# Performance work log

Hardware: AMD Instinct MI355X
Metric: run time of the kernel (lower is better)

The kernel has to match this reference:

```python
import jax, jax.numpy as jnp
import numpy as np
from jax import lax

B = 8192
NQ = 4  # num_qubits
TWO_PI = 2.0 * np.pi
BN_EPS = 1e-5
ANG_EPS = 1e-6


def setup_inputs() -> dict:
    key = jax.random.key(0)
    ks = jax.random.split(key, 8)
    rn = lambda k, shape, s: jax.random.normal(k, shape, jnp.float32) * s
    return {
        "x": jax.random.normal(ks[0], (B, 1, 28, 28), jnp.float32),
        "conv1_w": rn(ks[1], (8, 1, 3, 3), 0.3),
        "conv1_b": jnp.zeros((8,), jnp.float32),
        "conv2_w": rn(ks[2], (16, 8, 3, 3), 0.1),
        "conv2_b": jnp.zeros((16,), jnp.float32),
        "fc1_w": rn(ks[3], (64, 16 * 7 * 7), 0.04),
        "fc1_b": jnp.zeros((64,), jnp.float32),
        "fc2_w": rn(ks[4], (NQ, 64), 0.12),
        "fc2_b": jnp.zeros((NQ,), jnp.float32),
        "bn_gamma": jnp.ones((NQ,), jnp.float32),
        "bn_beta": jnp.zeros((NQ,), jnp.float32),
        "var_params": jax.random.uniform(ks[5], (3 * NQ,), jnp.float32, 0.0, TWO_PI),
    }


# ---- batched 4-qubit statevector simulation (replaces per-sample Aer loop) ----

def _rx(t):
    c, s = jnp.cos(t / 2), jnp.sin(t / 2)
    return jnp.stack([jnp.stack([c + 0j, -1j * s], -1),
                      jnp.stack([-1j * s, c + 0j], -1)], -2).astype(jnp.complex64)


def _ry(t):
    c, s = jnp.cos(t / 2), jnp.sin(t / 2)
    return jnp.stack([jnp.stack([c, -s], -1),
                      jnp.stack([s, c], -1)], -2).astype(jnp.complex64)


def _rz(t):
    p = jnp.exp(-0.5j * t.astype(jnp.complex64))
    z = jnp.zeros_like(p)
    return jnp.stack([jnp.stack([p, z], -1),
                      jnp.stack([z, jnp.conj(p)], -1)], -2)


def _apply_1q(psi, U, q):
    # psi: [B, 2,2,2,2]; axis q+1 is qubit q. U: [2,2] or [B,2,2].
    psi = jnp.moveaxis(psi, q + 1, 1)
    if U.ndim == 2:
        psi = jnp.einsum('ij,bj...->bi...', U, psi)
    else:
        psi = jnp.einsum('bij,bj...->bi...', U, psi)
    return jnp.moveaxis(psi, 1, q + 1)


def _apply_cnot(psi, c, t):
    ac, at = c + 1, t + 1
    c0 = lax.index_in_dim(psi, 0, ac, keepdims=True)
    c1 = jnp.flip(lax.index_in_dim(psi, 1, ac, keepdims=True), axis=at)
    return jnp.concatenate([c0, c1], axis=ac)


def quantum_expectations(angles, var):
    # angles: [B, NQ] feature angles; var: [3*NQ] shared variational params.
    b = angles.shape[0]
    psi = jnp.zeros((b,) + (2,) * NQ, jnp.complex64)
    psi = psi.at[(slice(None),) + (0,) * NQ].set(1.0)
    for i in range(NQ):                       # Z feature map
        psi = _apply_1q(psi, _rz(angles[:, i]), i)
    for i in range(NQ):                       # RX/RY/RZ ansatz
        psi = _apply_1q(psi, _rx(var[3 * i]), i)
        psi = _apply_1q(psi, _ry(var[3 * i + 1]), i)
        psi = _apply_1q(psi, _rz(var[3 * i + 2]), i)
    for i in range(NQ - 1):                   # linear CNOT chain
        psi = _apply_cnot(psi, i, i + 1)
    p = psi.real ** 2 + psi.imag ** 2          # [B,2,2,2,2] probabilities
    exps = []
    for k in range(NQ):                       # <Z> on qubit k
        axes = tuple(a for a in range(1, NQ + 1) if a != k + 1)
        pk = jnp.sum(p, axis=axes)             # [B,2]
        exps.append(pk[:, 0] - pk[:, 1])
    expZ = jnp.stack(exps, axis=1)             # [B,NQ], qubit-indexed
    # Qiskit Pauli label 'I'*q+'Z'+'I'*(NQ-q-1) puts Z on qubit NQ-1-q -> reverse
    return expZ[:, ::-1]


def _forward(x, conv1_w, conv1_b, conv2_w, conv2_b, fc1_w, fc1_b,
             fc2_w, fc2_b, bn_gamma, bn_beta, var_params):
    dn = ('NCHW', 'OIHW', 'NCHW')
    h = lax.conv_general_dilated(x, conv1_w, (1, 1), 'SAME', dimension_numbers=dn)
    h = jax.nn.relu(h + conv1_b[None, :, None, None])
    h = lax.reduce_window(h, -jnp.inf, lax.max, (1, 1, 2, 2), (1, 1, 2, 2), 'VALID')
    h = lax.conv_general_dilated(h, conv2_w, (1, 1), 'SAME', dimension_numbers=dn)
    h = jax.nn.relu(h + conv2_b[None, :, None, None])
    h = lax.reduce_window(h, -jnp.inf, lax.max, (1, 1, 2, 2), (1, 1, 2, 2), 'VALID')
    feats = h.reshape(h.shape[0], -1)                         # [B, 16*7*7]
    h = jax.nn.relu(feats @ fc1_w.T + fc1_b)
    logits = h @ fc2_w.T + fc2_b                              # [B, NQ]
    # BatchNorm1d (training mode: biased batch stats)
    mu = jnp.mean(logits, axis=0)
    var = jnp.mean((logits - mu) ** 2, axis=0)
    cl = (logits - mu) / jnp.sqrt(var + BN_EPS) * bn_gamma + bn_beta
    # quantum branch is fully detached in the original (numpy round-trip)
    cld = lax.stop_gradient(cl)
    mn = jnp.min(cld, axis=1, keepdims=True)
    mx = jnp.max(cld, axis=1, keepdims=True)
    angles = (cld - mn) / (mx - mn + ANG_EPS) * TWO_PI
    q = lax.stop_gradient(quantum_expectations(angles, var_params))
    return cl + q


def reference(x, conv1_w, conv1_b, conv2_w, conv2_b, fc1_w, fc1_b,
              fc2_w, fc2_b, bn_gamma, bn_beta, var_params):
    return _forward(x, conv1_w, conv1_b, conv2_w, conv2_b, fc1_w, fc1_b,
                    fc2_w, fc2_b, bn_gamma, bn_beta, var_params)
```

## Files before the change

kernel.cpp:

```cpp
#include <hip/hip_runtime.h>
#include <math.h>
#include <stdint.h>

#define BATCH 8192
#define NS 8

typedef _Float16 f16;
typedef _Float16 f16x2 __attribute__((ext_vector_type(2)));
typedef _Float16 f16x8 __attribute__((ext_vector_type(8)));
typedef float f32x4 __attribute__((ext_vector_type(4)));
typedef uint32_t u32x4 __attribute__((ext_vector_type(4)));

__device__ __forceinline__ uint32_t pk2(float a, float b) {
    return __builtin_bit_cast(uint32_t, __builtin_amdgcn_cvt_pkrtz(a, b));
}
__device__ __forceinline__ uint32_t rfl_u(uint32_t v) {
    return (uint32_t)__builtin_amdgcn_readfirstlane((int)v);
}
__device__ __forceinline__ void wave_lds_fence() {
    asm volatile("s_waitcnt lgkmcnt(0)" ::: "memory");
}

__global__ __launch_bounds__(512) void fused_cnn(
    const float* __restrict__ x,
    const float* __restrict__ c1w,
    const float* __restrict__ c1b,
    const float* __restrict__ c2w,
    const float* __restrict__ c2b,
    const float* __restrict__ f1w,
    const float* __restrict__ f1b,
    const float* __restrict__ f2w,
    const float* __restrict__ f2b,
    float* __restrict__ logits)
{
    const int tid  = threadIdx.x;
    const int lane = tid & 63;
    const int wid  = tid >> 6;
    const int b0   = blockIdx.x * NS;

    __shared__ __align__(16) f16 h1[NS * 16 * 18 * 8];
    __shared__ __align__(16) unsigned char uni[NS * 1920];
    float* part = (float*)h1;
    float* shl  = (float*)((unsigned char*)h1 + 4096);

    {
        uint4 z = make_uint4(0, 0, 0, 0);
        uint4* zs = (uint4*)(uni + wid * 1920);
        for (int i = lane; i < 120; i += 64) zs[i] = z;
        uint4* zh = (uint4*)(h1 + wid * 2304);
        for (int i = lane; i < 288; i += 64) zh[i] = z;
    }

    f16x2 wpk[36], bpk[4];
#pragma unroll
    for (int t = 0; t < 9; ++t)
#pragma unroll
        for (int pr = 0; pr < 4; ++pr)
            wpk[t * 4 + pr] = __builtin_bit_cast(f16x2,
                rfl_u(pk2(c1w[(2 * pr) * 9 + t], c1w[(2 * pr + 1) * 9 + t])));
#pragma unroll
    for (int pr = 0; pr < 4; ++pr)
        bpk[pr] = __builtin_bit_cast(f16x2, rfl_u(pk2(c1b[2 * pr], c1b[2 * pr + 1])));

    const int col = lane & 15, grp = lane >> 4;

    f16x8 af[3];
#pragma unroll
    for (int st = 0; st < 3; ++st) {
        int tap = st * 4 + grp;
        if (tap < 9) {
            float tmp[8];
#pragma unroll
            for (int j = 0; j < 8; ++j) tmp[j] = c2w[(col * 8 + j) * 9 + tap];
            u32x4 t = { pk2(tmp[0], tmp[1]), pk2(tmp[2], tmp[3]),
                        pk2(tmp[4], tmp[5]), pk2(tmp[6], tmp[7]) };
            af[st] = __builtin_bit_cast(f16x8, t);
        } else {
            u32x4 t = {0u, 0u, 0u, 0u};
            af[st] = __builtin_bit_cast(f16x8, t);
        }
    }

    {
        f16* simg = (f16*)(uni + wid * 1920);
        const float* xb = x + (size_t)(b0 + wid) * 784;
        wave_lds_fence();
#pragma unroll 1
        for (int pass = 0; pass < 4; ++pass) {
            int item = pass * 64 + lane;
            if (item < 196) {
                int r = item / 7, c4 = item - 7 * r;
                float4 v = *(const float4*)(xb + r * 28 + c4 * 4);
                f16* dst = simg + (r + 1) * 32 + c4 * 4 + 1;
                dst[0] = (f16)v.x; dst[1] = (f16)v.y;
                dst[2] = (f16)v.z; dst[3] = (f16)v.w;
            }
        }
    }
    wave_lds_fence();

    {
        const f16* simg = (const f16*)(uni + wid * 1920);
        f16* h1s = h1 + wid * 2304;
#pragma unroll 1
        for (int pass = 0; pass < 4; ++pass) {
            int pix = pass * 64 + lane;
            if (pix < 196) {
                int py = pix / 14, px = pix - 14 * py;
                const f16* ib = simg + (2 * py) * 32 + 2 * px;
                f16x2 acc[2][2][4];
#pragma unroll
                for (int qy = 0; qy < 2; ++qy)
#pragma unroll
                for (int qx = 0; qx < 2; ++qx)
#pragma unroll
                for (int pr = 0; pr < 4; ++pr) acc[qy][qx][pr] = bpk[pr];

#pragma unroll
                for (int rr = 0; rr < 4; ++rr) {
                    f16x2 plo = *(const f16x2*)(ib + rr * 32);
                    f16x2 phi = *(const f16x2*)(ib + rr * 32 + 2);
                    f16x2 sp[4];
                    sp[0][0] = plo[0]; sp[0][1] = plo[0];
                    sp[1][0] = plo[1]; sp[1][1] = plo[1];
                    sp[2][0] = phi[0]; sp[2][1] = phi[0];
                    sp[3][0] = phi[1]; sp[3][1] = phi[1];
#pragma unroll
                    for (int qy = 0; qy < 2; ++qy) {
                        int ky = rr - qy;
                        if (ky < 0 || ky > 2) continue;
#pragma unroll
                        for (int qx = 0; qx < 2; ++qx)
#pragma unroll
                        for (int kx = 0; kx < 3; ++kx) {
#pragma unroll
                            for (int pr = 0; pr < 4; ++pr)
                                acc[qy][qx][pr] = __builtin_elementwise_fma(
                                    sp[qx + kx], wpk[(ky * 3 + kx) * 4 + pr],
                                    acc[qy][qx][pr]);
                        }
                    }
                }
                f16x2 z; z[0] = (f16)0.f; z[1] = (f16)0.f;
                uint32_t ov[4];
#pragma unroll
                for (int pr = 0; pr < 4; ++pr) {
                    f16x2 m = __builtin_elementwise_max(
                        __builtin_elementwise_max(acc[0][0][pr], acc[0][1][pr]),
                        __builtin_elementwise_max(acc[1][0][pr], acc[1][1][pr]));
                    m = __builtin_elementwise_max(m, z);
                    ov[pr] = __builtin_bit_cast(uint32_t, m);
                }
                uint4 val = make_uint4(ov[0], ov[1], ov[2], ov[3]);
                *(uint4*)(h1s + ((py + 1) * 18 + (px + 1)) * 8) = val;
            }
        }
    }
    wave_lds_fence();

    {
        const f16* h1b = h1 + wid * 2304;
        f16* sfeats = (f16*)uni + wid * 968;
        const int q = col & 3, pl = col >> 2;
        const int qy = q >> 1, qx = q & 1;
        int koff[3];
#pragma unroll
        for (int st = 0; st < 3; ++st) {
            int t = st * 4 + grp;
            int ky = (t < 9) ? (t / 3) : 0;
            int kx = (t < 9) ? (t - 3 * (t / 3)) : 0;
            koff[st] = (ky * 18 + kx) * 8;
        }
        f32x4 cb;
#pragma unroll
        for (int r = 0; r < 4; ++r) cb[r] = c2b[grp * 4 + r];

#pragma unroll 1
        for (int t = 0; t < 13; ++t) {
            int pc = 4 * t + pl; pc = pc > 48 ? 48 : pc;
            int py = (pc * 9363) >> 16;
            int px = pc - 7 * py;
            const f16* bp = h1b + ((2 * py + qy) * 18 + (2 * px + qx)) * 8;
            f32x4 c = cb;
#pragma unroll
            for (int st = 0; st < 3; ++st) {
                f16x8 bv = *(const f16x8*)(bp + koff[st]);
                c = __builtin_amdgcn_mfma_f32_16x16x32_f16(af[st], bv, c, 0, 0, 0);
            }
            float vr[4];
#pragma unroll
            for (int r = 0; r < 4; ++r) {
                float v = c[r];
                v = fmaxf(v, __shfl_xor(v, 1));
                v = fmaxf(v, __shfl_xor(v, 2));
                vr[r] = fmaxf(v, 0.f);
            }
            int p = 4 * t + pl;
            if (q == 0 && p <= 48) {
#pragma unroll
                for (int r = 0; r < 4; ++r)
                    sfeats[(grp * 4 + r) * 49 + p] = (f16)vr[r];
            }
        }
        if (lane < 8) *(uint32_t*)(sfeats + 784 + lane * 2) = 0u;
    }
    __syncthreads();

    {
        const int rt = wid & 3, kh = wid >> 2;
        const int row = rt * 16 + col;
        const float* wrow = f1w + (size_t)row * 784;
        const int kbase = kh * 416;
        const int steps = 13 - kh;
        const int scol = col < NS ? col : 0;
        const f16* fb = (const f16*)uni + scol * 968;
        f32x4 c = {0.f, 0.f, 0.f, 0.f};
#pragma unroll 4
        for (int st = 0; st < steps; ++st) {
            int k0 = kbase + st * 32 + grp * 8;
            f16x8 a;
            if (k0 < 784) {
                float4 lo = *(const float4*)(wrow + k0);
                float4 hi = *(const float4*)(wrow + k0 + 4);
                u32x4 t = { pk2(lo.x, lo.y), pk2(lo.z, lo.w),
                            pk2(hi.x, hi.y), pk2(hi.z, hi.w) };
                a = __builtin_bit_cast(f16x8, t);
            } else {
                u32x4 t = {0u, 0u, 0u, 0u};
                a = __builtin_bit_cast(f16x8, t);
            }
            f16x8 b = *(const f16x8*)(fb + k0);
            c = __builtin_amdgcn_mfma_f32_16x16x32_f16(a, b, c, 0, 0, 0);
        }
        if (col < NS) {
#pragma unroll
            for (int r = 0; r < 4; ++r)
                part[kh * 512 + (rt * 16 + grp * 4 + r) * 8 + col] = c[r];
        }
    }
    __syncthreads();

    {
        const int m = tid >> 3, sm = tid & 7;
        float v = part[m * 8 + sm] + part[512 + m * 8 + sm] + f1b[m];
        shl[sm * 64 + m] = fmaxf(v, 0.f);
    }
    __syncthreads();

    {
        float hv = shl[wid * 64 + lane];
        float lg[4];
#pragma unroll
        for (int o = 0; o < 4; ++o) {
            float pv = hv * f2w[o * 64 + lane];
#pragma unroll
            for (int sft = 32; sft >= 1; sft >>= 1) pv += __shfl_xor(pv, sft);
            lg[o] = pv + f2b[o];
        }
        if (lane == 0) {
            float4 out4 = make_float4(lg[0], lg[1], lg[2], lg[3]);
            *(float4*)(logits + (size_t)(b0 + wid) * 4) = out4;
        }
    }
}

__global__ __launch_bounds__(256) void stats_apply(
    const float* __restrict__ logits, const float* __restrict__ var,
    const float* __restrict__ gamma, const float* __restrict__ beta,
    float* __restrict__ out)
{
    const int tid = threadIdx.x;
    const float4* l4 = (const float4*)logits;

    float t[8] = {0, 0, 0, 0, 0, 0, 0, 0};
#pragma unroll 4
    for (int i = 0; i < 32; ++i) {
        float4 v = l4[tid + 256 * i];
        t[0] += v.x; t[1] += v.y; t[2] += v.z; t[3] += v.w;
        t[4] += v.x * v.x; t[5] += v.y * v.y; t[6] += v.z * v.z; t[7] += v.w * v.w;
    }
#pragma unroll
    for (int sft = 32; sft >= 1; sft >>= 1)
#pragma unroll
        for (int j = 0; j < 8; ++j) t[j] += __shfl_xor(t[j], sft);

    __shared__ float part[4][8];
    __shared__ float prm[8];
    if ((tid & 63) == 0) {
#pragma unroll
        for (int j = 0; j < 8; ++j) part[tid >> 6][j] = t[j];
    }
    __syncthreads();

    if (tid == 0) {
        float sums[8];
#pragma unroll
        for (int j = 0; j < 8; ++j)
            sums[j] = part[0][j] + part[1][j] + part[2][j] + part[3][j];

        float pr[16], pi[16];
#pragma unroll
        for (int i = 0; i < 16; ++i) { pr[i] = 0.f; pi[i] = 0.f; }
        pr[0] = 1.f;
        for (int q = 0; q < 4; ++q) {
            float a  = var[3 * q], b_ = var[3 * q + 1], c = var[3 * q + 2];
            float ca = cosf(0.5f * a),  sa = sinf(0.5f * a);
            float cb = cosf(0.5f * b_), sb = sinf(0.5f * b_);
            float cc = cosf(0.5f * c),  sc = sinf(0.5f * c);
            float m00r = cb * ca, m00i =  sb * sa;
            float m01r = -sb * ca, m01i = -cb * sa;
            float m10r =  sb * ca, m10i = -cb * sa;
            float m11r =  cb * ca, m11i = -sb * sa;
            float u00r = cc * m00r + sc * m00i, u00i = cc * m00i - sc * m00r;
            float u01r = cc * m01r + sc * m01i, u01i = cc * m01i - sc * m01r;
            float u10r = cc * m10r - sc * m10i, u10i = cc * m10i + sc * m10r;
            float u11r = cc * m11r - sc * m11i, u11i = cc * m11i + sc * m11r;
            int stq = 1 << (3 - q);
            for (int i = 0; i < 16; ++i) {
                if (i & stq) continue;
                int j = i | stq;
                float xr = pr[i], xi = pi[i], yr = pr[j], yi = pi[j];
                pr[i] = u00r * xr - u00i * xi + u01r * yr - u01i * yi;
                pi[i] = u00r * xi + u00i * xr + u01r * yi + u01i * yr;
                pr[j] = u10r * xr - u10i * xi + u11r * yr - u11i * yi;
                pi[j] = u10r * xi + u10i * xr + u11r * yi + u11i * yr;
            }
        }
        for (int c = 0; c < 3; ++c) {
            int scm = 1 << (3 - c), stm = 1 << (2 - c);
            for (int i = 0; i < 16; ++i) {
                if ((i & scm) && !(i & stm)) {
                    int j = i | stm;
                    float tr = pr[i], ti = pi[i];
                    pr[i] = pr[j]; pi[i] = pi[j];
                    pr[j] = tr;    pi[j] = ti;
                }
            }
        }
        float p[16];
#pragma unroll
        for (int i = 0; i < 16; ++i) p[i] = pr[i] * pr[i] + pi[i] * pi[i];
        float e[4];
        for (int k = 0; k < 4; ++k) {
            float s = 0.f;
            for (int i = 0; i < 16; ++i)
                s += ((i >> (3 - k)) & 1) ? -p[i] : p[i];
            e[k] = s;
        }
        const float invB = 1.0f / (float)BATCH;
        for (int j = 0; j < 4; ++j) {
            float mu   = sums[j] * invB;
            float vr   = sums[4 + j] * invB - mu * mu;
            float istd = 1.0f / sqrtf(vr + 1e-5f);
            float scale = gamma[j] * istd;
            prm[j]     = scale;
            prm[4 + j] = beta[j] - mu * scale + e[3 - j];
        }
    }
    __syncthreads();

    const int smp = blockIdx.x * 256 + tid;
    float4 v = l4[smp];
    float4 r;
    r.x = v.x * prm[0] + prm[4];
    r.y = v.y * prm[1] + prm[5];
    r.z = v.z * prm[2] + prm[6];
    r.w = v.w * prm[3] + prm[7];
    ((float4*)out)[smp] = r;
}

extern "C" void kernel_launch(void* const* d_in, const int* in_sizes, int n_in,
                              void* d_out, int out_size, void* d_ws, size_t ws_size,
                              hipStream_t stream) {
    (void)in_sizes; (void)n_in; (void)out_size; (void)ws_size;
    const float* x   = (const float*)d_in[0];
    const float* c1w = (const float*)d_in[1];
    const float* c1b = (const float*)d_in[2];
    const float* c2w = (const float*)d_in[3];
    const float* c2b = (const float*)d_in[4];
    const float* f1w = (const float*)d_in[5];
    const float* f1b = (const float*)d_in[6];
    const float* f2w = (const float*)d_in[7];
    const float* f2b = (const float*)d_in[8];
    const float* gma = (const float*)d_in[9];
    const float* bta = (const float*)d_in[10];
    const float* var = (const float*)d_in[11];
    float* out = (float*)d_out;

    float* logits = (float*)d_ws;

    fused_cnn<<<BATCH / NS, 512, 0, stream>>>(x, c1w, c1b, c2w, c2b,
                                              f1w, f1b, f2w, f2b, logits);
    stats_apply<<<32, 256, 0, stream>>>(logits, var, gma, bta, out);
}
```

Before: 146.7 us.

## Prepack fc1 weights to fp16, halve samples per block, restructure conv2 pooling

Adds a small pre-kernel that converts fc1 weights to zero-padded fp16 once per call, so the fused kernel loads packed halves instead of converting fp32 on every block. The block shrinks to 4 samples and 256 threads, with an occupancy hint. Each wave now computes all 64 fc1 outputs for its row tile over the full K range, which removes the split-K partial buffer and one barrier. Conv2 now computes all four pooling quadrants per MFMA tile and takes the max in registers, replacing the cross-lane shuffles. Image staging is also widened to packed 32-bit stores. The trade-off is an extra kernel launch and fc1 weight reads repeated across twice as many blocks.

```diff
diff --git a/kernel.cpp b/kernel.cpp
--- a/kernel.cpp
+++ b/kernel.cpp
@@ -3,7 +3,7 @@
 #include <stdint.h>
 
 #define BATCH 8192
-#define NS 8
+#define NS 4
 
 typedef _Float16 f16;
 typedef _Float16 f16x2 __attribute__((ext_vector_type(2)));
@@ -21,13 +21,26 @@
     asm volatile("s_waitcnt lgkmcnt(0)" ::: "memory");
 }
 
-__global__ __launch_bounds__(512) void fused_cnn(
+__global__ __launch_bounds__(256) void pack_weights(
+    const float* __restrict__ f1w, uint32_t* __restrict__ w1p16)
+{
+    int idx = blockIdx.x * 256 + threadIdx.x;
+    if (idx < 25600) {
+        int o = idx / 400, pos = idx - o * 400;
+        int k0 = 2 * pos;
+        float v0 = (k0 < 784)     ? f1w[o * 784 + k0]     : 0.f;
+        float v1 = (k0 + 1 < 784) ? f1w[o * 784 + k0 + 1] : 0.f;
+        w1p16[idx] = pk2(v0, v1);
+    }
+}
+
+__global__ __launch_bounds__(256, 6) void fused_cnn(
     const float* __restrict__ x,
     const float* __restrict__ c1w,
     const float* __restrict__ c1b,
     const float* __restrict__ c2w,
     const float* __restrict__ c2b,
-    const float* __restrict__ f1w,
+    const f16* __restrict__ w1p16,
     const float* __restrict__ f1b,
     const float* __restrict__ f2w,
     const float* __restrict__ f2b,
@@ -39,14 +52,13 @@
     const int b0   = blockIdx.x * NS;
 
     __shared__ __align__(16) f16 h1[NS * 16 * 18 * 8];
-    __shared__ __align__(16) unsigned char uni[NS * 1920];
-    float* part = (float*)h1;
-    float* shl  = (float*)((unsigned char*)h1 + 4096);
+    __shared__ __align__(16) unsigned char uni[NS * 2048];
+    float* shl = (float*)h1;
 
     {
         uint4 z = make_uint4(0, 0, 0, 0);
-        uint4* zs = (uint4*)(uni + wid * 1920);
-        for (int i = lane; i < 120; i += 64) zs[i] = z;
+        uint4* zs = (uint4*)(uni + wid * 2048);
+        for (int i = lane; i < 128; i += 64) zs[i] = z;
         uint4* zh = (uint4*)(h1 + wid * 2304);
         for (int i = lane; i < 288; i += 64) zh[i] = z;
     }
@@ -65,10 +77,13 @@
     const int col = lane & 15, grp = lane >> 4;
 
     f16x8 af[3];
+    int koff[3];
 #pragma unroll
     for (int st = 0; st < 3; ++st) {
         int tap = st * 4 + grp;
         if (tap < 9) {
+            int ky = tap / 3, kx = tap - 3 * (tap / 3);
+            koff[st] = (ky * 18 + kx) * 8;
             float tmp[8];
 #pragma unroll
             for (int j = 0; j < 8; ++j) tmp[j] = c2w[(col * 8 + j) * 9 + tap];
@@ -76,38 +91,38 @@
                         pk2(tmp[4], tmp[5]), pk2(tmp[6], tmp[7]) };
             af[st] = __builtin_bit_cast(f16x8, t);
         } else {
+            koff[st] = 0;
             u32x4 t = {0u, 0u, 0u, 0u};
             af[st] = __builtin_bit_cast(f16x8, t);
         }
     }
-
-    {
-        f16* simg = (f16*)(uni + wid * 1920);
+    wave_lds_fence();
+
+    {
+        f16* simg = (f16*)(uni + wid * 2048);
         const float* xb = x + (size_t)(b0 + wid) * 784;
-        wave_lds_fence();
 #pragma unroll 1
         for (int pass = 0; pass < 4; ++pass) {
             int item = pass * 64 + lane;
             if (item < 196) {
                 int r = item / 7, c4 = item - 7 * r;
                 float4 v = *(const float4*)(xb + r * 28 + c4 * 4);
-                f16* dst = simg + (r + 1) * 32 + c4 * 4 + 1;
-                dst[0] = (f16)v.x; dst[1] = (f16)v.y;
-                dst[2] = (f16)v.z; dst[3] = (f16)v.w;
+                int off = (r + 1) * 32 + 2 + 4 * c4;
+                *(uint32_t*)(simg + off)     = pk2(v.x, v.y);
+                *(uint32_t*)(simg + off + 2) = pk2(v.z, v.w);
             }
         }
     }
     wave_lds_fence();
 
     {
-        const f16* simg = (const f16*)(uni + wid * 1920);
+        const f16* simg = (const f16*)(uni + wid * 2048);
         f16* h1s = h1 + wid * 2304;
 #pragma unroll 1
         for (int pass = 0; pass < 4; ++pass) {
             int pix = pass * 64 + lane;
             if (pix < 196) {
                 int py = pix / 14, px = pix - 14 * py;
-                const f16* ib = simg + (2 * py) * 32 + 2 * px;
                 f16x2 acc[2][2][4];
 #pragma unroll
                 for (int qy = 0; qy < 2; ++qy)
@@ -118,13 +133,14 @@
 
 #pragma unroll
                 for (int rr = 0; rr < 4; ++rr) {
-                    f16x2 plo = *(const f16x2*)(ib + rr * 32);
-                    f16x2 phi = *(const f16x2*)(ib + rr * 32 + 2);
+                    const f16* rb = simg + (2 * py + rr) * 32 + 2 * px;
+                    f16x2 A = *(const f16x2*)(rb);
+                    f16x2 Bv = *(const f16x2*)(rb + 2);
+                    f16x2 C = *(const f16x2*)(rb + 4);
+                    f16 P[4] = { A[1], Bv[0], Bv[1], C[0] };
                     f16x2 sp[4];
-                    sp[0][0] = plo[0]; sp[0][1] = plo[0];
-                    sp[1][0] = plo[1]; sp[1][1] = plo[1];
-                    sp[2][0] = phi[0]; sp[2][1] = phi[0];
-                    sp[3][0] = phi[1]; sp[3][1] = phi[1];
+#pragma unroll
+                    for (int i = 0; i < 4; ++i) { sp[i][0] = P[i]; sp[i][1] = P[i]; }
 #pragma unroll
                     for (int qy = 0; qy < 2; ++qy) {
                         int ky = rr - qy;
@@ -160,46 +176,33 @@
 
     {
         const f16* h1b = h1 + wid * 2304;
-        f16* sfeats = (f16*)uni + wid * 968;
-        const int q = col & 3, pl = col >> 2;
-        const int qy = q >> 1, qx = q & 1;
-        int koff[3];
-#pragma unroll
-        for (int st = 0; st < 3; ++st) {
-            int t = st * 4 + grp;
-            int ky = (t < 9) ? (t / 3) : 0;
-            int kx = (t < 9) ? (t - 3 * (t / 3)) : 0;
-            koff[st] = (ky * 18 + kx) * 8;
-        }
+        f16* sfeats = (f16*)(uni + wid * 2048);
         f32x4 cb;
 #pragma unroll
         for (int r = 0; r < 4; ++r) cb[r] = c2b[grp * 4 + r];
 
-#pragma unroll 1
-        for (int t = 0; t < 13; ++t) {
-            int pc = 4 * t + pl; pc = pc > 48 ? 48 : pc;
-            int py = (pc * 9363) >> 16;
-            int px = pc - 7 * py;
-            const f16* bp = h1b + ((2 * py + qy) * 18 + (2 * px + qx)) * 8;
-            f32x4 c = cb;
-#pragma unroll
-            for (int st = 0; st < 3; ++st) {
-                f16x8 bv = *(const f16x8*)(bp + koff[st]);
-                c = __builtin_amdgcn_mfma_f32_16x16x32_f16(af[st], bv, c, 0, 0, 0);
-            }
-            float vr[4];
-#pragma unroll
-            for (int r = 0; r < 4; ++r) {
-                float v = c[r];
-                v = fmaxf(v, __shfl_xor(v, 1));
-                v = fmaxf(v, __shfl_xor(v, 2));
-                vr[r] = fmaxf(v, 0.f);
-            }
-            int p = 4 * t + pl;
-            if (q == 0 && p <= 48) {
+#pragma unroll
+        for (int T = 0; T < 4; ++T) {
+            int p = 16 * T + col; p = p > 48 ? 48 : p;
+            int py = (p * 9363) >> 16;
+            int px = p - 7 * py;
+            const f16* base = h1b + (2 * py * 18 + 2 * px) * 8;
+            f32x4 vmax = {-1e30f, -1e30f, -1e30f, -1e30f};
+#pragma unroll
+            for (int q = 0; q < 4; ++q) {
+                const f16* bp = base + ((q >> 1) * 18 + (q & 1)) * 8;
+                f32x4 c = {0.f, 0.f, 0.f, 0.f};
+#pragma unroll
+                for (int st = 0; st < 3; ++st) {
+                    f16x8 bv = *(const f16x8*)(bp + koff[st]);
+                    c = __builtin_amdgcn_mfma_f32_16x16x32_f16(af[st], bv, c, 0, 0, 0);
+                }
+                vmax = __builtin_elementwise_max(vmax, c);
+            }
+            if (16 * T + col <= 48) {
 #pragma unroll
                 for (int r = 0; r < 4; ++r)
-                    sfeats[(grp * 4 + r) * 49 + p] = (f16)vr[r];
+                    sfeats[(grp * 4 + r) * 49 + p] = (f16)fmaxf(vmax[r] + cb[r], 0.f);
             }
         }
         if (lane < 8) *(uint32_t*)(sfeats + 784 + lane * 2) = 0u;
@@ -207,43 +210,26 @@
     __syncthreads();
 
     {
-        const int rt = wid & 3, kh = wid >> 2;
-        const int row = rt * 16 + col;
-        const float* wrow = f1w + (size_t)row * 784;
-        const int kbase = kh * 416;
-        const int steps = 13 - kh;
+        const f16* wrow = w1p16 + (size_t)(wid * 16 + col) * 800;
         const int scol = col < NS ? col : 0;
-        const f16* fb = (const f16*)uni + scol * 968;
+        const f16* fb = (const f16*)(uni + scol * 2048);
         f32x4 c = {0.f, 0.f, 0.f, 0.f};
-#pragma unroll 4
-        for (int st = 0; st < steps; ++st) {
-            int k0 = kbase + st * 32 + grp * 8;
-            f16x8 a;
-            if (k0 < 784) {
-                float4 lo = *(const float4*)(wrow + k0);
-                float4 hi = *(const float4*)(wrow + k0 + 4);
-                u32x4 t = { pk2(lo.x, lo.y), pk2(lo.z, lo.w),
-                            pk2(hi.x, hi.y), pk2(hi.z, hi.w) };
-                a = __builtin_bit_cast(f16x8, t);
-            } else {
-                u32x4 t = {0u, 0u, 0u, 0u};
-                a = __builtin_bit_cast(f16x8, t);
-            }
+#pragma unroll 5
+        for (int st = 0; st < 25; ++st) {
+            int k0 = st * 32 + grp * 8;
+            f16x8 a = *(const f16x8*)(wrow + k0);
             f16x8 b = *(const f16x8*)(fb + k0);
             c = __builtin_amdgcn_mfma_f32_16x16x32_f16(a, b, c, 0, 0, 0);
         }
         if (col < NS) {
-#pragma unroll
-            for (int r = 0; r < 4; ++r)
-                part[kh * 512 + (rt * 16 + grp * 4 + r) * 8 + col] = c[r];
-        }
-    }
-    __syncthreads();
-
-    {
-        const int m = tid >> 3, sm = tid & 7;
-        float v = part[m * 8 + sm] + part[512 + m * 8 + sm] + f1b[m];
-        shl[sm * 64 + m] = fmaxf(v, 0.f);
+            const int u0 = wid * 16 + grp * 4;
+            float4 h;
+            h.x = fmaxf(c[0] + f1b[u0 + 0], 0.f);
+            h.y = fmaxf(c[1] + f1b[u0 + 1], 0.f);
+            h.z = fmaxf(c[2] + f1b[u0 + 2], 0.f);
+            h.w = fmaxf(c[3] + f1b[u0 + 3], 0.f);
+            *(float4*)(shl + col * 64 + u0) = h;
+        }
     }
     __syncthreads();
 
@@ -387,9 +373,12 @@
     const float* var = (const float*)d_in[11];
     float* out = (float*)d_out;
 
-    float* logits = (float*)d_ws;
-
-    fused_cnn<<<BATCH / NS, 512, 0, stream>>>(x, c1w, c1b, c2w, c2b,
-                                              f1w, f1b, f2w, f2b, logits);
+    float*    logits = (float*)d_ws;
+    uint32_t* w1p16  = (uint32_t*)(logits + 32768);
+
+    pack_weights<<<100, 256, 0, stream>>>(f1w, w1p16);
+    fused_cnn<<<BATCH / NS, 256, 0, stream>>>(x, c1w, c1b, c2w, c2b,
+                                              (const f16*)w1p16, f1b, f2w, f2b,
+                                              logits);
     stats_apply<<<32, 256, 0, stream>>>(logits, var, gma, bta, out);
 }
```

After: 139.0 us. 1.06x faster.
